# Kernel tuning notes

Measured on AMD Instinct MI355X. Metric: run time of the kernel, lower is better.

## Reference

```python
import jax, jax.numpy as jnp
import numpy as np

N, D, K = 100000, 512, 1024

def setup_inputs() -> dict:
    key = jax.random.key(0)
    k1, k2 = jax.random.split(key)
    nodes = jax.random.normal(k1, (N, D), dtype=jnp.float32)
    # Faithful to original: indices sampled in [0, d) (torch.randint(d, ...))
    center_ind = jax.random.randint(k2, (K,), 0, D, dtype=jnp.int32)
    return {"nodes": nodes, "center_ind": center_ind, "num_clusters": K}


def reference(nodes, center_ind, num_clusters):
    # nodes: [n, d]; initial centers gathered from nodes (indices in [0, d) per original code)
    centers0 = nodes[center_ind]                      # [K, d]
    # Squared L2 distances via the expansion trick; avoids materializing [K, n, d].
    # argmin over squared distance == argmin over distance (sqrt is monotone).
    node_sq = jnp.sum(nodes * nodes, axis=1)          # [n]
    cent_sq = jnp.sum(centers0 * centers0, axis=1)    # [K]
    # d2[k, i] = ||c_k||^2 + ||x_i||^2 - 2 c_k . x_i
    d2 = cent_sq[:, None] + node_sq[None, :] - 2.0 * jnp.einsum("kd,nd->kn", centers0, nodes)
    assignment = jnp.argmin(d2, axis=0)               # [n]
    # Scatter-add nodes into their assigned cluster (index_add equivalent).
    centers = jax.ops.segment_sum(nodes, assignment, num_segments=num_clusters)  # [K, d]
    return centers
```

## Files before the change

kernel.cpp:

```cpp
#include <hip/hip_runtime.h>
#include <stdint.h>


typedef _Float16 f16x8  __attribute__((ext_vector_type(8)));
typedef float    f32x4  __attribute__((ext_vector_type(4)));

#define DD 512
#define KK 1024

static __device__ __forceinline__ unsigned orderable(float s) {
    unsigned u = __float_as_uint(s);
    return (u & 0x80000000u) ? ~u : (u | 0x80000000u);
}

static __device__ __forceinline__ void gload_lds16(const void* gsrc, void* ldst) {
    __builtin_amdgcn_global_load_lds(
        (const __attribute__((address_space(1))) unsigned int*)gsrc,
        (__attribute__((address_space(3))) unsigned int*)ldst, 16, 0, 0);
}

__global__ void canon_first(const int* __restrict__ center_ind,
                            unsigned* __restrict__ firstk, int K) {
    int k = (int)(blockIdx.x * blockDim.x + threadIdx.x);
    if (k < K) atomicMin(&firstk[center_ind[k]], (unsigned)k);
}
__global__ void canon_map(const int* __restrict__ center_ind,
                          const unsigned* __restrict__ firstk,
                          unsigned* __restrict__ canon, int K) {
    int k = (int)(blockIdx.x * blockDim.x + threadIdx.x);
    if (k < K) canon[k] = firstk[center_ind[k]];
}

__global__ void gather_centers(const float* __restrict__ nodes,
                               const int* __restrict__ center_ind,
                               _Float16* __restrict__ centf,
                               float* __restrict__ cent_sq,
                               int K) {
    int k    = (int)blockIdx.x;
    int lane = (int)threadIdx.x;
    int ci   = center_ind[k];
    const f32x4* p = reinterpret_cast<const f32x4*>(nodes + (size_t)ci * DD + lane * 8);
    f32x4 v0 = p[0], v1 = p[1];
    f16x8 h;
    h[0]=(_Float16)v0[0]; h[1]=(_Float16)v0[1]; h[2]=(_Float16)v0[2]; h[3]=(_Float16)v0[3];
    h[4]=(_Float16)v1[0]; h[5]=(_Float16)v1[1]; h[6]=(_Float16)v1[2]; h[7]=(_Float16)v1[3];
    int t = k >> 4, r = k & 15;
    *reinterpret_cast<f16x8*>(centf + ((size_t)((t * 64 + lane) * 16 + r) << 3)) = h;
    float ssq = v0[0]*v0[0]+v0[1]*v0[1]+v0[2]*v0[2]+v0[3]*v0[3]
              + v1[0]*v1[0]+v1[1]*v1[1]+v1[2]*v1[2]+v1[3]*v1[3];
    #pragma unroll
    for (int off = 32; off > 0; off >>= 1) ssq += __shfl_xor(ssq, off, 64);
    if (lane == 0) cent_sq[k] = ssq;
}

__launch_bounds__(256, 2)
__global__ void assign_mfma(const float* __restrict__ nodes,
                            const _Float16* __restrict__ centf,
                            const float* __restrict__ cent_sq,
                            unsigned long long* __restrict__ bestg,
                            int N, int K) {
    __shared__ __align__(16) _Float16 nt[64 * DD];
    __shared__ __align__(16) _Float16 ab[2][4096];

    const int tid = (int)threadIdx.x;
    const int n0  = (int)blockIdx.x * 64;
    const int lane = tid & 63;
    const int wid  = tid >> 6;

    #pragma unroll
    for (int it = 0; it < 16; ++it) {
        int f   = it * 256 + tid;
        int row = f >> 6;
        int d0  = (f & 63) << 3;
        f32x4 v0 = {0.f,0.f,0.f,0.f}, v1 = {0.f,0.f,0.f,0.f};
        if (n0 + row < N) {
            const f32x4* p = reinterpret_cast<const f32x4*>(nodes + (size_t)(n0 + row) * DD + d0);
            v0 = p[0]; v1 = p[1];
        }
        f16x8 h;
        h[0]=(_Float16)v0[0]; h[1]=(_Float16)v0[1]; h[2]=(_Float16)v0[2]; h[3]=(_Float16)v0[3];
        h[4]=(_Float16)v1[0]; h[5]=(_Float16)v1[1]; h[6]=(_Float16)v1[2]; h[7]=(_Float16)v1[3];
        int byte = ((row << 10) + (d0 << 1)) ^ ((row & 7) << 4);
        *reinterpret_cast<f16x8*>(reinterpret_cast<char*>(nt) + byte) = h;
    }

    const int l15 = lane & 15;
    const int g   = lane >> 4;
    const int swz = (l15 & 7) << 4;
    char* ntb = reinterpret_cast<char*>(nt);
    const char* cfb = reinterpret_cast<const char*>(centf);

    int bbase[4];
    #pragma unroll
    for (int nG = 0; nG < 4; ++nG) bbase[nG] = (((nG * 16 + l15) << 10) + (g << 4));

    #define STAGE(buf_, gs_)                                                         \
        { const int ct_ = (gs_) >> 4, s_ = (gs_) & 15;                               \
          _Pragma("unroll")                                                          \
          for (int i_ = 0; i_ < 2; ++i_) {                                           \
              const int c_ = i_ * 4 + wid;                                           \
              gload_lds16(cfb + (size_t)(ct_ * 8 + c_) * 16384                       \
                              + (size_t)s_ * 1024 + lane * 16,                       \
                          reinterpret_cast<char*>(&ab[buf_][0]) + c_ * 1024);        \
          } }
    #define LB(dst, s_)                                                             \
        { _Pragma("unroll")                                                          \
          for (int nG = 0; nG < 4; ++nG)                                             \
              dst[nG] = *reinterpret_cast<const f16x8*>(                             \
                  ntb + ((bbase[nG] + ((s_) << 6)) ^ swz)); }

    f32x4 acc[2][4];
    #pragma unroll
    for (int a = 0; a < 2; ++a)
        #pragma unroll
        for (int b = 0; b < 4; ++b) { f32x4 z = {0.f,0.f,0.f,0.f}; acc[a][b] = z; }
    unsigned long long pk[4] = {~0ULL, ~0ULL, ~0ULL, ~0ULL};

    STAGE(0, 0);
    __syncthreads();

    for (int ct = 0; ct < 8; ++ct) {
        #pragma unroll
        for (int s = 0; s < 16; ++s) {
            const int gs = ct * 16 + s;
            if (gs + 1 < 128) STAGE((gs + 1) & 1, gs + 1);
            const char* abb = reinterpret_cast<const char*>(&ab[gs & 1][0]);
            f16x8 Afr[2], Bfr[4];
            #pragma unroll
            for (int t = 0; t < 2; ++t)
                Afr[t] = *reinterpret_cast<const f16x8*>(
                    abb + ((2 * wid + t) << 10) + (lane << 4));
            LB(Bfr, s);
            #pragma unroll
            for (int t = 0; t < 2; ++t)
                #pragma unroll
                for (int nG = 0; nG < 4; ++nG)
                    acc[t][nG] = __builtin_amdgcn_mfma_f32_16x16x32_f16(
                        Afr[t], Bfr[nG], acc[t][nG], 0, 0, 0);
            __syncthreads();
        }

        #pragma unroll
        for (int tC = 0; tC < 2; ++tC) {
            const int cb = ct * 128 + wid * 32 + tC * 16 + g * 4;
            f32x4 cs = *reinterpret_cast<const f32x4*>(cent_sq + cb);
            #pragma unroll
            for (int nG = 0; nG < 4; ++nG) {
                #pragma unroll
                for (int q = 0; q < 4; ++q) {
                    float sc = fmaf(-2.f, acc[tC][nG][q], cs[q]);
                    unsigned long long v =
                        ((unsigned long long)orderable(sc) << 32) | (unsigned)(cb + q);
                    pk[nG] = v < pk[nG] ? v : pk[nG];
                }
            }
        }
        #pragma unroll
        for (int a = 0; a < 2; ++a)
            #pragma unroll
            for (int b = 0; b < 4; ++b) { f32x4 z = {0.f,0.f,0.f,0.f}; acc[a][b] = z; }
    }
    #undef STAGE
    #undef LB

    #pragma unroll
    for (int nG = 0; nG < 4; ++nG) {
        unsigned long long p = pk[nG], o;
        o = __shfl_xor(p, 16, 64); p = o < p ? o : p;
        o = __shfl_xor(p, 32, 64); p = o < p ? o : p;
        int n = n0 + nG * 16 + l15;
        if (lane < 16 && n < N) atomicMin(&bestg[n], p);
    }
}

__global__ void finalize(const unsigned long long* __restrict__ bestg,
                         const unsigned* __restrict__ canon,
                         unsigned* __restrict__ assignment,
                         unsigned* __restrict__ counts, int N) {
    int i = (int)(blockIdx.x * blockDim.x + threadIdx.x);
    if (i < N) {
        unsigned k = canon[(unsigned)(bestg[i] & 0xffffffffu)];
        assignment[i] = k;
        atomicAdd(&counts[k], 1u);
    }
}

__global__ void scan_offsets(const unsigned* __restrict__ counts,
                             unsigned* __restrict__ cursor) {
    __shared__ unsigned s[KK];
    int t = (int)threadIdx.x;
    unsigned c = counts[t];
    s[t] = c;
    __syncthreads();
    for (int off = 1; off < KK; off <<= 1) {
        unsigned v = (t >= off) ? s[t - off] : 0u;
        __syncthreads();
        s[t] += v;
        __syncthreads();
    }
    cursor[t] = s[t] - c;
}

__global__ void scatter_idx(const unsigned* __restrict__ assignment,
                            unsigned* __restrict__ cursor,
                            unsigned* __restrict__ keys, int N) {
    int i = (int)(blockIdx.x * blockDim.x + threadIdx.x);
    if (i < N) {
        unsigned k = assignment[i];
        unsigned slot = atomicAdd(&cursor[k], 1u);
        keys[slot] = (k << 20) | (unsigned)i;
    }
}

#define CHUNK 32
__launch_bounds__(256, 4)
__global__ void aggregate3(const float* __restrict__ nodes,
                           const unsigned* __restrict__ keys,
                           float* __restrict__ out, int N) {
    const int tid  = (int)threadIdx.x;
    const int wid  = tid >> 6;
    const int lane = tid & 63;
    const int base = ((int)blockIdx.x * 4 + wid) * CHUNK;
    if (base >= N) return;
    const int n    = min(CHUNK, N - base);

    int sI = base + (lane & 31);
    unsigned myk = (sI < N) ? keys[sI] : 0u;

    f32x4 a0 = {0.f,0.f,0.f,0.f}, a1 = {0.f,0.f,0.f,0.f};
    int curk = -1;
    auto flush = [&](void) {
        float* dst = out + ((size_t)curk << 9) + lane * 8;
        #pragma unroll
        for (int e = 0; e < 4; ++e) atomicAdd(dst + e, a0[e]);
        #pragma unroll
        for (int e = 0; e < 4; ++e) atomicAdd(dst + 4 + e, a1[e]);
    };

    int j = 0;
    while (j < n) {
        int b = n - j; if (b > 4) b = 4;
        f32x4 r[4][2];
        int   kk[4];
        #pragma unroll
        for (int t = 0; t < 4; ++t) {
            if (t < b) {
                unsigned key = __shfl(myk, j + t, 64);
                kk[t] = (int)(key >> 20);
                const f32x4* p = reinterpret_cast<const f32x4*>(
                    nodes + ((size_t)(key & 0xFFFFFu) << 9) + lane * 8);
                r[t][0] = p[0];
                r[t][1] = p[1];
            }
        }
        #pragma unroll
        for (int t = 0; t < 4; ++t) {
            if (t < b) {
                if (kk[t] != curk) {
                    if (curk >= 0) flush();
                    curk = kk[t];
                    f32x4 z = {0.f,0.f,0.f,0.f}; a0 = z; a1 = z;
                }
                a0 += r[t][0];
                a1 += r[t][1];
            }
        }
        j += 4;
    }
    if (curk >= 0) flush();
}

extern "C" void kernel_launch(void* const* d_in, const int* in_sizes, int n_in,
                              void* d_out, int out_size, void* d_ws, size_t ws_size,
                              hipStream_t stream) {
    const float* nodes      = (const float*)d_in[0];
    const int*   center_ind = (const int*)d_in[1];
    int K = in_sizes[1];
    int D = out_size / K;
    int N = in_sizes[0] / D;

    char* ws = (char*)d_ws;
    _Float16* centf      = (_Float16*)ws;
    size_t    o          = (size_t)K * DD * 2;
    float*    cent_sq    = (float*)(ws + o);    o += (size_t)K * 4;
    unsigned* assignment = (unsigned*)(ws + o); o += (size_t)N * 4;
    unsigned* counts     = (unsigned*)(ws + o); o += (size_t)K * 4;
    unsigned* cursor     = (unsigned*)(ws + o); o += (size_t)K * 4;
    unsigned* firstk     = (unsigned*)(ws + o); o += (size_t)D * 4;
    unsigned* canon      = (unsigned*)(ws + o); o += (size_t)K * 4;
    unsigned* keys       = (unsigned*)(ws + o); o += (size_t)N * 4;
    o = (o + 7) & ~(size_t)7;
    unsigned long long* bestg = (unsigned long long*)(ws + o); o += (size_t)N * 8;
    float*    out        = (float*)d_out;

    hipMemsetAsync(counts, 0, (size_t)K * sizeof(unsigned), stream);
    hipMemsetAsync(firstk, 0xFF, (size_t)D * sizeof(unsigned), stream);
    hipMemsetAsync(bestg, 0xFF, (size_t)N * sizeof(unsigned long long), stream);
    hipMemsetAsync(out, 0, (size_t)out_size * sizeof(float), stream);

    canon_first<<<(K + 255) / 256, 256, 0, stream>>>(center_ind, firstk, K);
    canon_map<<<(K + 255) / 256, 256, 0, stream>>>(center_ind, firstk, canon, K);
    gather_centers<<<K, 64, 0, stream>>>(nodes, center_ind, centf, cent_sq, K);
    assign_mfma<<<(N + 63) / 64, 256, 0, stream>>>(nodes, centf, cent_sq, bestg, N, K);
    finalize<<<(N + 255) / 256, 256, 0, stream>>>(bestg, canon, assignment, counts, N);
    scan_offsets<<<1, KK, 0, stream>>>(counts, cursor);
    scatter_idx<<<(N + 255) / 256, 256, 0, stream>>>(assignment, cursor, keys, N);
    aggregate3<<<(N + 4 * CHUNK - 1) / (4 * CHUNK), 256, 0, stream>>>(nodes, keys, out, N);
}
```

Before: 579.0 us.

## Deepen center-tile prefetch to four LDS buffers and shrink node tile to 48

Changes the assign kernel's center staging from double-buffered to a 4-slot ring with three tiles in flight. It swaps __syncthreads for an explicit vmcnt wait plus raw barriers, and raises wave priority around the MFMA block. The node tile per block drops from 64 to 48 rows, which cuts LDS per block and raises the block count, but each center tile is reused across fewer nodes, so global center traffic grows. The aim is to hide global-to-LDS latency and raise occupancy. The hand-written waitcnt depends on the compiler's load ordering, and the loop issues dummy loads at the tail.

Result: slower. 598.2 us (+3.3%).

```diff
diff --git a/kernel.cpp b/kernel.cpp
--- a/kernel.cpp
+++ b/kernel.cpp
@@ -7,6 +7,7 @@
 
 #define DD 512
 #define KK 1024
+#define NT 48
 
 static __device__ __forceinline__ unsigned orderable(float s) {
     unsigned u = __float_as_uint(s);
@@ -59,16 +60,16 @@
                             const float* __restrict__ cent_sq,
                             unsigned long long* __restrict__ bestg,
                             int N, int K) {
-    __shared__ __align__(16) _Float16 nt[64 * DD];
-    __shared__ __align__(16) _Float16 ab[2][4096];
+    __shared__ __align__(16) _Float16 nt[NT * DD];
+    __shared__ __align__(16) _Float16 ab[4][4096];
 
     const int tid = (int)threadIdx.x;
-    const int n0  = (int)blockIdx.x * 64;
+    const int n0  = (int)blockIdx.x * NT;
     const int lane = tid & 63;
     const int wid  = tid >> 6;
 
     #pragma unroll
-    for (int it = 0; it < 16; ++it) {
+    for (int it = 0; it < 12; ++it) {
         int f   = it * 256 + tid;
         int row = f >> 6;
         int d0  = (f & 63) << 3;
@@ -90,9 +91,9 @@
     char* ntb = reinterpret_cast<char*>(nt);
     const char* cfb = reinterpret_cast<const char*>(centf);
 
-    int bbase[4];
-    #pragma unroll
-    for (int nG = 0; nG < 4; ++nG) bbase[nG] = (((nG * 16 + l15) << 10) + (g << 4));
+    int bbase[3];
+    #pragma unroll
+    for (int nG = 0; nG < 3; ++nG) bbase[nG] = (((nG * 16 + l15) << 10) + (g << 4));
 
     #define STAGE(buf_, gs_)                                                         \
         { const int ct_ = (gs_) >> 4, s_ = (gs_) & 15;                               \
@@ -103,41 +104,51 @@
                               + (size_t)s_ * 1024 + lane * 16,                       \
                           reinterpret_cast<char*>(&ab[buf_][0]) + c_ * 1024);        \
           } }
-    #define LB(dst, s_)                                                             \
-        { _Pragma("unroll")                                                          \
-          for (int nG = 0; nG < 4; ++nG)                                             \
-              dst[nG] = *reinterpret_cast<const f16x8*>(                             \
-                  ntb + ((bbase[nG] + ((s_) << 6)) ^ swz)); }
-
-    f32x4 acc[2][4];
+
+    f32x4 acc[2][3];
     #pragma unroll
     for (int a = 0; a < 2; ++a)
         #pragma unroll
-        for (int b = 0; b < 4; ++b) { f32x4 z = {0.f,0.f,0.f,0.f}; acc[a][b] = z; }
-    unsigned long long pk[4] = {~0ULL, ~0ULL, ~0ULL, ~0ULL};
-
-    STAGE(0, 0);
+        for (int b = 0; b < 3; ++b) { f32x4 z = {0.f,0.f,0.f,0.f}; acc[a][b] = z; }
+    unsigned long long pk[3] = {~0ULL, ~0ULL, ~0ULL};
+
+    STAGE(0, 0); STAGE(1, 1); STAGE(2, 2);
     __syncthreads();
 
     for (int ct = 0; ct < 8; ++ct) {
         #pragma unroll
         for (int s = 0; s < 16; ++s) {
             const int gs = ct * 16 + s;
-            if (gs + 1 < 128) STAGE((gs + 1) & 1, gs + 1);
-            const char* abb = reinterpret_cast<const char*>(&ab[gs & 1][0]);
-            f16x8 Afr[2], Bfr[4];
+            {
+                const int nx  = gs + 3;
+                const int gsx = (nx < 128) ? nx : 0;
+                STAGE((s + 3) & 3, gsx);
+            }
+            asm volatile("s_waitcnt vmcnt(6)" ::: "memory");
+            __builtin_amdgcn_s_barrier();
+            __builtin_amdgcn_sched_barrier(0);
+
+            const char* abb = reinterpret_cast<const char*>(&ab[s & 3][0]);
+            f16x8 Afr[2], Bfr[3];
             #pragma unroll
             for (int t = 0; t < 2; ++t)
                 Afr[t] = *reinterpret_cast<const f16x8*>(
                     abb + ((2 * wid + t) << 10) + (lane << 4));
-            LB(Bfr, s);
+            #pragma unroll
+            for (int nG = 0; nG < 3; ++nG)
+                Bfr[nG] = *reinterpret_cast<const f16x8*>(
+                    ntb + ((bbase[nG] + (s << 6)) ^ swz));
+
+            __builtin_amdgcn_s_setprio(1);
             #pragma unroll
             for (int t = 0; t < 2; ++t)
                 #pragma unroll
-                for (int nG = 0; nG < 4; ++nG)
+                for (int nG = 0; nG < 3; ++nG)
                     acc[t][nG] = __builtin_amdgcn_mfma_f32_16x16x32_f16(
                         Afr[t], Bfr[nG], acc[t][nG], 0, 0, 0);
-            __syncthreads();
+            __builtin_amdgcn_s_setprio(0);
+            __builtin_amdgcn_sched_barrier(0);
+            __builtin_amdgcn_s_barrier();
         }
 
         #pragma unroll
@@ -145,7 +156,7 @@
             const int cb = ct * 128 + wid * 32 + tC * 16 + g * 4;
             f32x4 cs = *reinterpret_cast<const f32x4*>(cent_sq + cb);
             #pragma unroll
-            for (int nG = 0; nG < 4; ++nG) {
+            for (int nG = 0; nG < 3; ++nG) {
                 #pragma unroll
                 for (int q = 0; q < 4; ++q) {
                     float sc = fmaf(-2.f, acc[tC][nG][q], cs[q]);
@@ -158,13 +169,12 @@
         #pragma unroll
         for (int a = 0; a < 2; ++a)
             #pragma unroll
-            for (int b = 0; b < 4; ++b) { f32x4 z = {0.f,0.f,0.f,0.f}; acc[a][b] = z; }
+            for (int b = 0; b < 3; ++b) { f32x4 z = {0.f,0.f,0.f,0.f}; acc[a][b] = z; }
     }
     #undef STAGE
-    #undef LB
-
-    #pragma unroll
-    for (int nG = 0; nG < 4; ++nG) {
+
+    #pragma unroll
+    for (int nG = 0; nG < 3; ++nG) {
         unsigned long long p = pk[nG], o;
         o = __shfl_xor(p, 16, 64); p = o < p ? o : p;
         o = __shfl_xor(p, 32, 64); p = o < p ? o : p;
@@ -301,7 +311,7 @@
     canon_first<<<(K + 255) / 256, 256, 0, stream>>>(center_ind, firstk, K);
     canon_map<<<(K + 255) / 256, 256, 0, stream>>>(center_ind, firstk, canon, K);
     gather_centers<<<K, 64, 0, stream>>>(nodes, center_ind, centf, cent_sq, K);
-    assign_mfma<<<(N + 63) / 64, 256, 0, stream>>>(nodes, centf, cent_sq, bestg, N, K);
+    assign_mfma<<<(N + NT - 1) / NT, 256, 0, stream>>>(nodes, centf, cent_sq, bestg, N, K);
     finalize<<<(N + 255) / 256, 256, 0, stream>>>(bestg, canon, assignment, counts, N);
     scan_offsets<<<1, KK, 0, stream>>>(counts, cursor);
     scatter_idx<<<(N + 255) / 256, 256, 0, stream>>>(assignment, cursor, keys, N);
```

## Retile assignment GEMM into 128x128 node-by-center tiles with small LDS

Applied to the files above, without the earlier changes.

The assignment kernel changes from one block per 64 nodes looping over all 1024 centers to a 2D grid of 128-node by 128-center tiles. Each block now streams both operands along D in 16 steps: node rows are converted to fp16 per step and centers are loaded directly into LDS. Per-block argmin results merge through global atomicMin. The much smaller LDS footprint and the higher launch-bounds occupancy target are meant to raise occupancy and MFMA density per wave. In exchange, each node is re-read and re-converted 8 times (once per center block), atomic traffic increases, and there is no double buffering, so each step waits on two barriers.

Result: faster. 562.0 us (-2.9%).

```diff
diff --git a/kernel.cpp b/kernel.cpp
--- a/kernel.cpp
+++ b/kernel.cpp
@@ -53,122 +53,108 @@
     if (lane == 0) cent_sq[k] = ssq;
 }
 
-__launch_bounds__(256, 2)
+__launch_bounds__(256, 3)
 __global__ void assign_mfma(const float* __restrict__ nodes,
                             const _Float16* __restrict__ centf,
                             const float* __restrict__ cent_sq,
                             unsigned long long* __restrict__ bestg,
                             int N, int K) {
-    __shared__ __align__(16) _Float16 nt[64 * DD];
-    __shared__ __align__(16) _Float16 ab[2][4096];
-
-    const int tid = (int)threadIdx.x;
-    const int n0  = (int)blockIdx.x * 64;
+    __shared__ __align__(16) _Float16 aT[8 * 512];
+    __shared__ __align__(16) _Float16 bT[4 * 1024];
+
+    const int tid  = (int)threadIdx.x;
     const int lane = tid & 63;
     const int wid  = tid >> 6;
-
-    #pragma unroll
-    for (int it = 0; it < 16; ++it) {
-        int f   = it * 256 + tid;
-        int row = f >> 6;
-        int d0  = (f & 63) << 3;
-        f32x4 v0 = {0.f,0.f,0.f,0.f}, v1 = {0.f,0.f,0.f,0.f};
-        if (n0 + row < N) {
-            const f32x4* p = reinterpret_cast<const f32x4*>(nodes + (size_t)(n0 + row) * DD + d0);
-            v0 = p[0]; v1 = p[1];
-        }
-        f16x8 h;
-        h[0]=(_Float16)v0[0]; h[1]=(_Float16)v0[1]; h[2]=(_Float16)v0[2]; h[3]=(_Float16)v0[3];
-        h[4]=(_Float16)v1[0]; h[5]=(_Float16)v1[1]; h[6]=(_Float16)v1[2]; h[7]=(_Float16)v1[3];
-        int byte = ((row << 10) + (d0 << 1)) ^ ((row & 7) << 4);
-        *reinterpret_cast<f16x8*>(reinterpret_cast<char*>(nt) + byte) = h;
-    }
-
-    const int l15 = lane & 15;
-    const int g   = lane >> 4;
-    const int swz = (l15 & 7) << 4;
-    char* ntb = reinterpret_cast<char*>(nt);
+    const int l15  = lane & 15;
+    const int g    = lane >> 4;
+    const int nblk = (int)blockIdx.x >> 3;
+    const int cblk = (int)blockIdx.x & 7;
+    const int n0   = nblk * 128;
+    const int c0   = cblk * 128;
+    const int w_n  = wid & 1;
+    const int w_c  = wid >> 1;
+
+    const int nn = tid >> 1;
+    const int j0 = (tid & 1) * 2;
+    const int gn = n0 + nn;
+    const bool valid = gn < N;
+    const f32x4* bp = reinterpret_cast<const f32x4*>(nodes + (size_t)gn * DD + j0 * 8);
+
+    char* aB = reinterpret_cast<char*>(aT);
+    char* bB = reinterpret_cast<char*>(bT);
     const char* cfb = reinterpret_cast<const char*>(centf);
-
-    int bbase[4];
-    #pragma unroll
-    for (int nG = 0; nG < 4; ++nG) bbase[nG] = (((nG * 16 + l15) << 10) + (g << 4));
-
-    #define STAGE(buf_, gs_)                                                         \
-        { const int ct_ = (gs_) >> 4, s_ = (gs_) & 15;                               \
-          _Pragma("unroll")                                                          \
-          for (int i_ = 0; i_ < 2; ++i_) {                                           \
-              const int c_ = i_ * 4 + wid;                                           \
-              gload_lds16(cfb + (size_t)(ct_ * 8 + c_) * 16384                       \
-                              + (size_t)s_ * 1024 + lane * 16,                       \
-                          reinterpret_cast<char*>(&ab[buf_][0]) + c_ * 1024);        \
-          } }
-    #define LB(dst, s_)                                                             \
-        { _Pragma("unroll")                                                          \
-          for (int nG = 0; nG < 4; ++nG)                                             \
-              dst[nG] = *reinterpret_cast<const f16x8*>(                             \
-                  ntb + ((bbase[nG] + ((s_) << 6)) ^ swz)); }
-
-    f32x4 acc[2][4];
-    #pragma unroll
-    for (int a = 0; a < 2; ++a)
+    const size_t asrc0 = (size_t)(c0 >> 4) * 16384;
+    const int ta = 2 * wid, tb = 2 * wid + 1;
+
+    f32x4 acc[4][4];
+    #pragma unroll
+    for (int a = 0; a < 4; ++a)
         #pragma unroll
         for (int b = 0; b < 4; ++b) { f32x4 z = {0.f,0.f,0.f,0.f}; acc[a][b] = z; }
+
+    for (int s = 0; s < 16; ++s) {
+        f32x4 v0 = {0.f,0.f,0.f,0.f}, v1 = v0, v2 = v0, v3 = v0;
+        if (valid) { v0 = bp[s*8]; v1 = bp[s*8+1]; v2 = bp[s*8+2]; v3 = bp[s*8+3]; }
+
+        __syncthreads();
+
+        f16x8 h0, h1;
+        h0[0]=(_Float16)v0[0]; h0[1]=(_Float16)v0[1]; h0[2]=(_Float16)v0[2]; h0[3]=(_Float16)v0[3];
+        h0[4]=(_Float16)v1[0]; h0[5]=(_Float16)v1[1]; h0[6]=(_Float16)v1[2]; h0[7]=(_Float16)v1[3];
+        h1[0]=(_Float16)v2[0]; h1[1]=(_Float16)v2[1]; h1[2]=(_Float16)v2[2]; h1[3]=(_Float16)v2[3];
+        h1[4]=(_Float16)v3[0]; h1[5]=(_Float16)v3[1]; h1[6]=(_Float16)v3[2]; h1[7]=(_Float16)v3[3];
+        *reinterpret_cast<f16x8*>(bB + (j0     << 11) + (nn << 4)) = h0;
+        *reinterpret_cast<f16x8*>(bB + ((j0+1) << 11) + (nn << 4)) = h1;
+
+        gload_lds16(cfb + asrc0 + (size_t)ta * 16384 + (size_t)s * 1024 + lane * 16,
+                    aB + ta * 1024);
+        gload_lds16(cfb + asrc0 + (size_t)tb * 16384 + (size_t)s * 1024 + lane * 16,
+                    aB + tb * 1024);
+
+        __syncthreads();
+
+        f16x8 Afr[4], Bfr[4];
+        #pragma unroll
+        for (int tC = 0; tC < 4; ++tC)
+            Afr[tC] = *reinterpret_cast<const f16x8*>(
+                aB + ((w_c * 4 + tC) << 10) + (lane << 4));
+        #pragma unroll
+        for (int nG = 0; nG < 4; ++nG)
+            Bfr[nG] = *reinterpret_cast<const f16x8*>(
+                bB + (g << 11) + ((w_n * 64 + nG * 16 + l15) << 4));
+
+        __builtin_amdgcn_s_setprio(1);
+        #pragma unroll
+        for (int tC = 0; tC < 4; ++tC)
+            #pragma unroll
+            for (int nG = 0; nG < 4; ++nG)
+                acc[tC][nG] = __builtin_amdgcn_mfma_f32_16x16x32_f16(
+                    Afr[tC], Bfr[nG], acc[tC][nG], 0, 0, 0);
+        __builtin_amdgcn_s_setprio(0);
+    }
+
     unsigned long long pk[4] = {~0ULL, ~0ULL, ~0ULL, ~0ULL};
-
-    STAGE(0, 0);
-    __syncthreads();
-
-    for (int ct = 0; ct < 8; ++ct) {
-        #pragma unroll
-        for (int s = 0; s < 16; ++s) {
-            const int gs = ct * 16 + s;
-            if (gs + 1 < 128) STAGE((gs + 1) & 1, gs + 1);
-            const char* abb = reinterpret_cast<const char*>(&ab[gs & 1][0]);
-            f16x8 Afr[2], Bfr[4];
+    #pragma unroll
+    for (int tC = 0; tC < 4; ++tC) {
+        const int cb = c0 + w_c * 64 + tC * 16 + g * 4;
+        f32x4 cs = *reinterpret_cast<const f32x4*>(cent_sq + cb);
+        #pragma unroll
+        for (int nG = 0; nG < 4; ++nG) {
             #pragma unroll
-            for (int t = 0; t < 2; ++t)
-                Afr[t] = *reinterpret_cast<const f16x8*>(
-                    abb + ((2 * wid + t) << 10) + (lane << 4));
-            LB(Bfr, s);
-            #pragma unroll
-            for (int t = 0; t < 2; ++t)
-                #pragma unroll
-                for (int nG = 0; nG < 4; ++nG)
-                    acc[t][nG] = __builtin_amdgcn_mfma_f32_16x16x32_f16(
-                        Afr[t], Bfr[nG], acc[t][nG], 0, 0, 0);
-            __syncthreads();
-        }
-
-        #pragma unroll
-        for (int tC = 0; tC < 2; ++tC) {
-            const int cb = ct * 128 + wid * 32 + tC * 16 + g * 4;
-            f32x4 cs = *reinterpret_cast<const f32x4*>(cent_sq + cb);
-            #pragma unroll
-            for (int nG = 0; nG < 4; ++nG) {
-                #pragma unroll
-                for (int q = 0; q < 4; ++q) {
-                    float sc = fmaf(-2.f, acc[tC][nG][q], cs[q]);
-                    unsigned long long v =
-                        ((unsigned long long)orderable(sc) << 32) | (unsigned)(cb + q);
-                    pk[nG] = v < pk[nG] ? v : pk[nG];
-                }
+            for (int q = 0; q < 4; ++q) {
+                float sc = fmaf(-2.f, acc[tC][nG][q], cs[q]);
+                unsigned long long v =
+                    ((unsigned long long)orderable(sc) << 32) | (unsigned)(cb + q);
+                pk[nG] = v < pk[nG] ? v : pk[nG];
             }
         }
-        #pragma unroll
-        for (int a = 0; a < 2; ++a)
-            #pragma unroll
-            for (int b = 0; b < 4; ++b) { f32x4 z = {0.f,0.f,0.f,0.f}; acc[a][b] = z; }
-    }
-    #undef STAGE
-    #undef LB
-
+    }
     #pragma unroll
     for (int nG = 0; nG < 4; ++nG) {
         unsigned long long p = pk[nG], o;
         o = __shfl_xor(p, 16, 64); p = o < p ? o : p;
         o = __shfl_xor(p, 32, 64); p = o < p ? o : p;
-        int n = n0 + nG * 16 + l15;
+        int n = n0 + w_n * 64 + nG * 16 + l15;
         if (lane < 16 && n < N) atomicMin(&bestg[n], p);
     }
 }
@@ -301,7 +287,10 @@
     canon_first<<<(K + 255) / 256, 256, 0, stream>>>(center_ind, firstk, K);
     canon_map<<<(K + 255) / 256, 256, 0, stream>>>(center_ind, firstk, canon, K);
     gather_centers<<<K, 64, 0, stream>>>(nodes, center_ind, centf, cent_sq, K);
-    assign_mfma<<<(N + 63) / 64, 256, 0, stream>>>(nodes, centf, cent_sq, bestg, N, K);
+
+    int nblk = (N + 127) / 128;
+    assign_mfma<<<nblk * 8, 256, 0, stream>>>(nodes, centf, cent_sq, bestg, N, K);
+
     finalize<<<(N + 255) / 256, 256, 0, stream>>>(bestg, canon, assignment, counts, N);
     scan_offsets<<<1, KK, 0, stream>>>(counts, cursor);
     scatter_idx<<<(N + 255) / 256, 256, 0, stream>>>(assignment, cursor, keys, N);
```
